# Optimization experiments

Hardware: AMD Instinct MI355X
Metric: run time of the kernel (lower is better)

Reference implementation:

```python
import jax, jax.numpy as jnp
import numpy as np

N_NODES = 50000
N_EDGES = 800000
IN_DIM = 128
IN_CH = 64
HIDDEN = 64
OUT_CH = 128
NUM_CLS = 16
NUM_GRAPHS = 512


def setup_inputs() -> dict:
    key = jax.random.key(0)
    ks = jax.random.split(key, 16)
    s = 0.02
    x = jax.random.normal(ks[0], (N_NODES, IN_DIM), jnp.float32)
    edge_index = jax.random.randint(ks[1], (2, N_EDGES), 0, N_NODES, jnp.int64)
    batch = jnp.sort(jax.random.randint(ks[2], (N_NODES,), 0, NUM_GRAPHS, jnp.int64))
    return {
        "x": x,
        "edge_index": edge_index,
        "batch": batch,
        "num_graphs": NUM_GRAPHS,
        "w_stage1": jax.random.normal(ks[3], (IN_DIM, IN_CH), jnp.float32) * s,
        "b_stage1": jnp.zeros((IN_CH,), jnp.float32),
        "rel1_w": jax.random.normal(ks[4], (IN_CH, HIDDEN), jnp.float32) * s,
        "rel1_b": jnp.zeros((HIDDEN,), jnp.float32),
        "root1_w": jax.random.normal(ks[5], (IN_CH, HIDDEN), jnp.float32) * s,
        "rel2_w": jax.random.normal(ks[6], (HIDDEN, 2 * HIDDEN), jnp.float32) * s,
        "rel2_b": jnp.zeros((2 * HIDDEN,), jnp.float32),
        "root2_w": jax.random.normal(ks[7], (HIDDEN, 2 * HIDDEN), jnp.float32) * s,
        "rel3_w": jax.random.normal(ks[8], (2 * HIDDEN, OUT_CH), jnp.float32) * s,
        "rel3_b": jnp.zeros((OUT_CH,), jnp.float32),
        "root3_w": jax.random.normal(ks[9], (2 * HIDDEN, OUT_CH), jnp.float32) * s,
        "lin_w": jax.random.normal(ks[10], (OUT_CH, NUM_CLS), jnp.float32) * s,
        "lin_b": jnp.zeros((NUM_CLS,), jnp.float32),
    }


def graph_conv(x, src, dst, rel_w, rel_b, root_w, n_nodes):
    # PyG GraphConv(aggr='add'): lin_rel(sum_{j in N(i)} x_j) + lin_root(x_i)
    agg = jax.ops.segment_sum(x[src], dst, num_segments=n_nodes)  # [N, in]
    return agg @ rel_w + rel_b + x @ root_w


def reference(x, edge_index, batch, num_graphs,
              w_stage1, b_stage1,
              rel1_w, rel1_b, root1_w,
              rel2_w, rel2_b, root2_w,
              rel3_w, rel3_b, root3_w,
              lin_w, lin_b):
    src, dst = edge_index[0], edge_index[1]
    n = x.shape[0]
    h = x @ w_stage1 + b_stage1                                   # [N, IN_CH]
    h = jax.nn.relu(graph_conv(h, src, dst, rel1_w, rel1_b, root1_w, n))
    h = jax.nn.relu(graph_conv(h, src, dst, rel2_w, rel2_b, root2_w, n))
    h = jax.nn.relu(graph_conv(h, src, dst, rel3_w, rel3_b, root3_w, n))
    # global mean pool over graphs
    sums = jax.ops.segment_sum(h, batch, num_segments=num_graphs)  # [G, OUT_CH]
    cnt = jax.ops.segment_sum(jnp.ones((n,), h.dtype), batch, num_segments=num_graphs)
    pooled = sums / jnp.maximum(cnt, 1.0)[:, None]
    # dropout treated as identity (deterministic eval reference)
    return pooled @ lin_w + lin_b                                  # [G, NUM_CLS]
```

## Files before the change

kernel.cpp:

```cpp
#include <hip/hip_runtime.h>
#include <hip/hip_bf16.h>

#define N_NODES 50000
#define N_EDGES 800000
#define IN_DIM  128
#define IN_CH   64
#define HIDDEN  64
#define OUT_CH  128
#define NUM_CLS 16
#define NUM_G   512
#define NBUK    ((N_NODES + 255) >> 8)
#define BCAP    6144
#define EPB_A   4096

typedef __attribute__((ext_vector_type(8))) short short8;
typedef __attribute__((ext_vector_type(4))) float f32x4;

__device__ inline float bits2f(unsigned short u) {
  unsigned x = (unsigned)u << 16;
  float f;
  __builtin_memcpy(&f, &x, 4);
  return f;
}
__device__ inline unsigned short f2bits(float v) {
  __hip_bfloat16 b = __float2bfloat16(v);
  unsigned short s;
  __builtin_memcpy(&s, &b, 2);
  return s;
}
__device__ inline short8 zero8() {
  short8 z;
#pragma unroll
  for (int i = 0; i < 8; ++i) z[i] = 0;
  return z;
}
__device__ inline void acc2(float& a0, float& a1, unsigned v) {
  a0 += bits2f((unsigned short)v);
  a1 += bits2f((unsigned short)(v >> 16));
}
__device__ inline void accu4(float* a, uint4 v) {
  acc2(a[0], a[1], v.x); acc2(a[2], a[3], v.y);
  acc2(a[4], a[5], v.z); acc2(a[6], a[7], v.w);
}

__global__ __launch_bounds__(64) void k_stage1(
    const float* __restrict__ Ap, const short* __restrict__ Wa,
    const float* __restrict__ bias, unsigned short* __restrict__ outp) {
  constexpr int DIN = 128, DOUT = 64, KT = DIN / 32, CT = DOUT / 16;
  const int lane = threadIdx.x;
  const int m = lane & 15;
  const int q = lane >> 4;
  const int row = blockIdx.x * 16 + m;
  const bool ok = row < N_NODES;

  short8 afr[KT];
#pragma unroll
  for (int kt = 0; kt < KT; ++kt) {
    short8 f = zero8();
    if (ok) {
      const float* ap = Ap + (size_t)row * DIN + kt * 32 + q * 8;
      float4 x0 = *(const float4*)ap;
      float4 x1 = *(const float4*)(ap + 4);
      f[0] = (short)f2bits(x0.x); f[1] = (short)f2bits(x0.y);
      f[2] = (short)f2bits(x0.z); f[3] = (short)f2bits(x0.w);
      f[4] = (short)f2bits(x1.x); f[5] = (short)f2bits(x1.y);
      f[6] = (short)f2bits(x1.z); f[7] = (short)f2bits(x1.w);
    }
    afr[kt] = f;
  }
  const int rbase = blockIdx.x * 16;
#pragma unroll
  for (int ct = 0; ct < CT; ++ct) {
    f32x4 c = {0.f, 0.f, 0.f, 0.f};
#pragma unroll
    for (int kt = 0; kt < KT; ++kt) {
      short8 b = *(const short8*)(Wa + ((size_t)(kt * CT + ct) * 64 + lane) * 8);
      c = __builtin_amdgcn_mfma_f32_16x16x32_bf16(afr[kt], b, c, 0, 0, 0);
    }
    float bv = bias[ct * 16 + m];
#pragma unroll
    for (int r = 0; r < 4; ++r) {
      int ro = rbase + q * 4 + r;
      if (ro < N_NODES) outp[(size_t)ro * DOUT + ct * 16 + m] = f2bits(c[r] + bv);
    }
  }
}

template <int DIN, int DOUT>
__global__ __launch_bounds__(64) void k_fused(
    const unsigned short* __restrict__ h, const int* __restrict__ esrc,
    const int* __restrict__ off, const short* __restrict__ Wa,
    const short* __restrict__ Wh, const float* __restrict__ bias,
    unsigned short* __restrict__ outp) {
  constexpr int KT = DIN / 32;
  constexpr int CT = DOUT / 16;
  const int lane = threadIdx.x;
  const int m = lane & 15;
  const int q = lane >> 4;
  const int node = blockIdx.x * 16 + m;
  const bool ok = node < N_NODES;

  float acc[KT][8];
#pragma unroll
  for (int kt = 0; kt < KT; ++kt)
#pragma unroll
    for (int j = 0; j < 8; ++j) acc[kt][j] = 0.f;

  if (ok) {
    int e = off[node], end = off[node + 1];
    const unsigned short* hq = h + q * 8;
    for (; e + 2 <= end; e += 2) {
      int s0 = esrc[e], s1 = esrc[e + 1];
      const unsigned short* r0 = hq + (size_t)s0 * DIN;
      const unsigned short* r1 = hq + (size_t)s1 * DIN;
#pragma unroll
      for (int kt = 0; kt < KT; ++kt) {
        uint4 va = *(const uint4*)(r0 + kt * 32);
        uint4 vb = *(const uint4*)(r1 + kt * 32);
        accu4(acc[kt], va);
        accu4(acc[kt], vb);
      }
    }
    if (e < end) {
      const unsigned short* r0 = hq + (size_t)esrc[e] * DIN;
#pragma unroll
      for (int kt = 0; kt < KT; ++kt)
        accu4(acc[kt], *(const uint4*)(r0 + kt * 32));
    }
  }

  short8 afr[KT], hfr[KT];
#pragma unroll
  for (int kt = 0; kt < KT; ++kt) {
    short8 f;
#pragma unroll
    for (int j = 0; j < 8; ++j) f[j] = (short)f2bits(acc[kt][j]);
    afr[kt] = f;
    hfr[kt] = ok ? *(const short8*)(h + (size_t)node * DIN + kt * 32 + q * 8)
                 : zero8();
  }

  const int rbase = blockIdx.x * 16;
#pragma unroll
  for (int ct = 0; ct < CT; ++ct) {
    f32x4 c = {0.f, 0.f, 0.f, 0.f};
#pragma unroll
    for (int kt = 0; kt < KT; ++kt) {
      short8 b = *(const short8*)(Wa + ((size_t)(kt * CT + ct) * 64 + lane) * 8);
      c = __builtin_amdgcn_mfma_f32_16x16x32_bf16(afr[kt], b, c, 0, 0, 0);
      short8 bh = *(const short8*)(Wh + ((size_t)(kt * CT + ct) * 64 + lane) * 8);
      c = __builtin_amdgcn_mfma_f32_16x16x32_bf16(hfr[kt], bh, c, 0, 0, 0);
    }
    float bv = bias[ct * 16 + m];
#pragma unroll
    for (int r = 0; r < 4; ++r) {
      int row = rbase + q * 4 + r;
      if (row < N_NODES)
        outp[(size_t)row * DOUT + ct * 16 + m] = f2bits(fmaxf(c[r] + bv, 0.f));
    }
  }
}

template <int DIN, int DOUT>
__device__ inline void pack1(const float* __restrict__ W, short* __restrict__ o,
                             int t) {
  constexpr int CT = DOUT / 16;
  int j = t & 7;
  int lane = (t >> 3) & 63;
  int kc = t >> 9;
  int ct = kc % CT;
  int kt = kc / CT;
  int k = kt * 32 + (lane >> 4) * 8 + j;
  int n = ct * 16 + (lane & 15);
  o[t] = (short)f2bits(W[k * DOUT + n]);
}

struct PackArgs {
  const float *w1, *r1, *o1, *r2, *o2, *r3, *o3;
  short *w1p, *r1p, *o1p, *r2p, *o2p, *r3p, *o3p;
};

__device__ inline void packflat(const PackArgs& a, int t) {
  if      (t < 8192)  pack1<128, 64>(a.w1, a.w1p, t);
  else if (t < 12288) pack1<64, 64>(a.r1, a.r1p, t - 8192);
  else if (t < 16384) pack1<64, 64>(a.o1, a.o1p, t - 12288);
  else if (t < 24576) pack1<64, 128>(a.r2, a.r2p, t - 16384);
  else if (t < 32768) pack1<64, 128>(a.o2, a.o2p, t - 24576);
  else if (t < 49152) pack1<128, 128>(a.r3, a.r3p, t - 32768);
  else if (t < 65536) pack1<128, 128>(a.o3, a.o3p, t - 49152);
}

__global__ __launch_bounds__(256) void k_bucketA(const int* __restrict__ src,
    const int* __restrict__ dst, int* __restrict__ bcnt, uint2* __restrict__ bbuf,
    PackArgs pk) {
  __shared__ int hist[NBUK], sbase[NBUK], lcur[NBUK];
  const int t = threadIdx.x;

  {
    int g0 = blockIdx.x * 256 + t;
    packflat(pk, g0);
    packflat(pk, g0 + 50176);
  }

  for (int i = t; i < NBUK; i += 256) { hist[i] = 0; lcur[i] = 0; }
  __syncthreads();
  const int e0 = blockIdx.x * EPB_A;
  int s_[16], d_[16];
  int cnt = 0;
#pragma unroll
  for (int k = 0; k < 16; ++k) {
    int e = e0 + k * 256 + t;
    if (e < N_EDGES) {
      s_[cnt] = src[e]; d_[cnt] = dst[e];
      atomicAdd(&hist[d_[cnt] >> 8], 1);
      cnt++;
    }
  }
  __syncthreads();
  for (int i = t; i < NBUK; i += 256) sbase[i] = atomicAdd(&bcnt[i], hist[i]);
  __syncthreads();
  for (int k = 0; k < cnt; ++k) {
    int b = d_[k] >> 8;
    int pos = sbase[b] + atomicAdd(&lcur[b], 1);
    if (pos < BCAP) bbuf[(size_t)b * BCAP + pos] = make_uint2((unsigned)s_[k], (unsigned)d_[k]);
  }
}

__global__ __launch_bounds__(256) void k_bfin(const int* __restrict__ bcnt,
    const uint2* __restrict__ bbuf, int* __restrict__ off,
    int* __restrict__ esrc) {
  __shared__ int cnt[256], s[256], soff[256];
  const int b = blockIdx.x;
  const int t = threadIdx.x;

  int bv0 = (t < NBUK) ? min(bcnt[t], BCAP) : 0;
  s[t] = bv0;
  __syncthreads();
  for (int st = 1; st < 256; st <<= 1) {
    int v = (t >= st) ? s[t - st] : 0;
    __syncthreads();
    s[t] += v;
    __syncthreads();
  }
  __shared__ int bbase_s;
  if (t == b) bbase_s = s[t] - bv0;
  if (b == 0 && t == NBUK - 1) off[N_NODES] = s[t];
  __syncthreads();
  const int bb = bbase_s;

  cnt[t] = 0;
  __syncthreads();
  int n = min(bcnt[b], BCAP);
  for (int i = t; i < n; i += 256)
    atomicAdd(&cnt[bbuf[(size_t)b * BCAP + i].y & 255], 1);
  __syncthreads();
  int v0 = cnt[t];
  s[t] = v0;
  __syncthreads();
  for (int st = 1; st < 256; st <<= 1) {
    int v = (t >= st) ? s[t - st] : 0;
    __syncthreads();
    s[t] += v;
    __syncthreads();
  }
  int myoff = bb + s[t] - v0;
  int node = b * 256 + t;
  if (node < N_NODES) off[node] = myoff;
  soff[t] = myoff;
  cnt[t] = 0;
  __syncthreads();
  for (int i = t; i < n; i += 256) {
    uint2 p = bbuf[(size_t)b * BCAP + i];
    int l = p.y & 255;
    int r = atomicAdd(&cnt[l], 1);
    esrc[soff[l] + r] = (int)p.x;
  }
}

__device__ inline int lbound(const int* __restrict__ a, int n, int v) {
  int lo = 0, hi = n;
  while (lo < hi) {
    int m = (lo + hi) >> 1;
    if (a[m] < v) lo = m + 1; else hi = m;
  }
  return lo;
}

__global__ __launch_bounds__(128) void k_poolhead(const unsigned short* __restrict__ h3,
    const int* __restrict__ batch, const float* __restrict__ lw,
    const float* __restrict__ lb, float* __restrict__ out) {
  __shared__ float sp[128];
  int g = blockIdx.x;
  int t = threadIdx.x;
  int lo = lbound(batch, N_NODES, g);
  int hi = lbound(batch, N_NODES, g + 1);
  float a0 = 0.f, a1 = 0.f, a2 = 0.f, a3 = 0.f;
  int r = lo;
  for (; r + 4 <= hi; r += 4) {
    a0 += bits2f(h3[(size_t)(r + 0) * OUT_CH + t]);
    a1 += bits2f(h3[(size_t)(r + 1) * OUT_CH + t]);
    a2 += bits2f(h3[(size_t)(r + 2) * OUT_CH + t]);
    a3 += bits2f(h3[(size_t)(r + 3) * OUT_CH + t]);
  }
  for (; r < hi; ++r) a0 += bits2f(h3[(size_t)r * OUT_CH + t]);
  float inv = (hi > lo) ? 1.f / (float)(hi - lo) : 0.f;
  sp[t] = ((a0 + a1) + (a2 + a3)) * inv;
  __syncthreads();
  if (t < NUM_CLS) {
    float s = lb[t];
#pragma unroll
    for (int k = 0; k < OUT_CH; ++k) s = fmaf(sp[k], lw[k * NUM_CLS + t], s);
    out[g * NUM_CLS + t] = s;
  }
}

extern "C" void kernel_launch(void* const* d_in, const int* in_sizes, int n_in,
                              void* d_out, int out_size, void* d_ws, size_t ws_size,
                              hipStream_t stream) {
  const float* x      = (const float*)d_in[0];
  const int*   ei     = (const int*)d_in[1];
  const int*   batch  = (const int*)d_in[2];
  const float* w1     = (const float*)d_in[4];
  const float* b1     = (const float*)d_in[5];
  const float* rel1w  = (const float*)d_in[6];
  const float* rel1b  = (const float*)d_in[7];
  const float* root1w = (const float*)d_in[8];
  const float* rel2w  = (const float*)d_in[9];
  const float* rel2b  = (const float*)d_in[10];
  const float* root2w = (const float*)d_in[11];
  const float* rel3w  = (const float*)d_in[12];
  const float* rel3b  = (const float*)d_in[13];
  const float* root3w = (const float*)d_in[14];
  const float* linw   = (const float*)d_in[15];
  const float* linb   = (const float*)d_in[16];
  const int* src = ei;
  const int* dst = ei + N_EDGES;
  float* out = (float*)d_out;

  unsigned short* P = (unsigned short*)d_ws;
  unsigned short* Q = P + (size_t)N_NODES * 128;
  unsigned short* R = Q + (size_t)N_NODES * 128;
  short* WP = (short*)(R + (size_t)N_NODES * 128);
  short* w1p  = WP;
  short* r1p  = w1p + 8192;
  short* o1p  = r1p + 4096;
  short* r2p  = o1p + 4096;
  short* o2p  = r2p + 8192;
  short* r3p  = o2p + 8192;
  short* o3p  = r3p + 16384;
  int* off     = (int*)(o3p + 16384);
  int* bcnt    = off + (N_NODES + 1);
  int* esrc    = bcnt + NBUK + 3;
  uint2* bbuf  = (uint2*)((char*)(esrc + N_EDGES) +
                          ((16 - (((size_t)(esrc + N_EDGES)) & 15)) & 15));

  PackArgs pk = {w1, rel1w, root1w, rel2w, root2w, rel3w, root3w,
                 w1p, r1p, o1p, r2p, o2p, r3p, o3p};

  hipMemsetAsync(bcnt, 0, NBUK * sizeof(int), stream);
  k_bucketA<<<(N_EDGES + EPB_A - 1) / EPB_A, 256, 0, stream>>>(src, dst, bcnt,
                                                               bbuf, pk);
  k_bfin<<<NBUK, 256, 0, stream>>>(bcnt, bbuf, off, esrc);

  const int GF = (N_NODES + 15) / 16;

  k_stage1<<<GF, 64, 0, stream>>>(x, w1p, b1, P);
  k_fused<64, 64><<<GF, 64, 0, stream>>>(P, esrc, off, r1p, o1p, rel1b, R);
  k_fused<64, 128><<<GF, 64, 0, stream>>>(R, esrc, off, r2p, o2p, rel2b, Q);
  k_fused<128, 128><<<GF, 64, 0, stream>>>(Q, esrc, off, r3p, o3p, rel3b, P);
  k_poolhead<<<NUM_G, 128, 0, stream>>>(P, batch, linw, linb, out);
}
```

Measured before the change: 250.5 us.

## Sort nodes by in-degree so GraphConv waves process similar-degree nodes

Adds a degree histogram in k_bfin and a new k_dsort kernel that builds a permutation of nodes ordered by in-degree, in descending order. The fused GraphConv kernels now take their 16 nodes per wave from this permutation and write outputs to the permuted rows. This is meant to cut lane divergence in the neighbor-gather loop, where a wave runs as long as its highest-degree node. In exchange it adds an extra kernel launch and atomics, and it makes the root-feature loads and output stores scattered instead of contiguous.

```diff
diff --git a/kernel.cpp b/kernel.cpp
--- a/kernel.cpp
+++ b/kernel.cpp
@@ -89,16 +89,15 @@
 template <int DIN, int DOUT>
 __global__ __launch_bounds__(64) void k_fused(
     const unsigned short* __restrict__ h, const int* __restrict__ esrc,
-    const int* __restrict__ off, const short* __restrict__ Wa,
-    const short* __restrict__ Wh, const float* __restrict__ bias,
-    unsigned short* __restrict__ outp) {
+    const int* __restrict__ off, const int* __restrict__ perm,
+    const short* __restrict__ Wa, const short* __restrict__ Wh,
+    const float* __restrict__ bias, unsigned short* __restrict__ outp) {
   constexpr int KT = DIN / 32;
   constexpr int CT = DOUT / 16;
   const int lane = threadIdx.x;
   const int m = lane & 15;
   const int q = lane >> 4;
-  const int node = blockIdx.x * 16 + m;
-  const bool ok = node < N_NODES;
+  const int node = perm[blockIdx.x * 16 + m];
 
   float acc[KT][8];
 #pragma unroll
@@ -106,7 +105,7 @@
 #pragma unroll
     for (int j = 0; j < 8; ++j) acc[kt][j] = 0.f;
 
-  if (ok) {
+  {
     int e = off[node], end = off[node + 1];
     const unsigned short* hq = h + q * 8;
     for (; e + 2 <= end; e += 2) {
@@ -136,11 +135,13 @@
 #pragma unroll
     for (int j = 0; j < 8; ++j) f[j] = (short)f2bits(acc[kt][j]);
     afr[kt] = f;
-    hfr[kt] = ok ? *(const short8*)(h + (size_t)node * DIN + kt * 32 + q * 8)
-                 : zero8();
+    hfr[kt] = *(const short8*)(h + (size_t)node * DIN + kt * 32 + q * 8);
   }
 
   const int rbase = blockIdx.x * 16;
+  int prow[4];
+#pragma unroll
+  for (int r = 0; r < 4; ++r) prow[r] = perm[rbase + q * 4 + r];
 #pragma unroll
   for (int ct = 0; ct < CT; ++ct) {
     f32x4 c = {0.f, 0.f, 0.f, 0.f};
@@ -154,9 +155,7 @@
     float bv = bias[ct * 16 + m];
 #pragma unroll
     for (int r = 0; r < 4; ++r) {
-      int row = rbase + q * 4 + r;
-      if (row < N_NODES)
-        outp[(size_t)row * DOUT + ct * 16 + m] = f2bits(fmaxf(c[r] + bv, 0.f));
+      outp[(size_t)prow[r] * DOUT + ct * 16 + m] = f2bits(fmaxf(c[r] + bv, 0.f));
     }
   }
 }
@@ -228,7 +227,7 @@
 
 __global__ __launch_bounds__(256) void k_bfin(const int* __restrict__ bcnt,
     const uint2* __restrict__ bbuf, int* __restrict__ off,
-    int* __restrict__ esrc) {
+    int* __restrict__ esrc, int* __restrict__ ghist) {
   __shared__ int cnt[256], s[256], soff[256];
   const int b = blockIdx.x;
   const int t = threadIdx.x;
@@ -265,7 +264,10 @@
   }
   int myoff = bb + s[t] - v0;
   int node = b * 256 + t;
-  if (node < N_NODES) off[node] = myoff;
+  if (node < N_NODES) {
+    off[node] = myoff;
+    atomicAdd(&ghist[v0 < 255 ? v0 : 255], 1);
+  }
   soff[t] = myoff;
   cnt[t] = 0;
   __syncthreads();
@@ -274,6 +276,29 @@
     int l = p.y & 255;
     int r = atomicAdd(&cnt[l], 1);
     esrc[soff[l] + r] = (int)p.x;
+  }
+}
+
+__global__ __launch_bounds__(256) void k_dsort(const int* __restrict__ off,
+    const int* __restrict__ ghist, int* __restrict__ gcur,
+    int* __restrict__ perm) {
+  __shared__ int s[256];
+  const int t = threadIdx.x;
+  s[t] = ghist[t];
+  __syncthreads();
+  for (int st = 1; st < 256; st <<= 1) {
+    int v = (t + st < 256) ? s[t + st] : 0;
+    __syncthreads();
+    s[t] += v;
+    __syncthreads();
+  }
+  int nid = blockIdx.x * 256 + t;
+  if (nid < N_NODES) {
+    int d = off[nid + 1] - off[nid];
+    if (d > 255) d = 255;
+    int base = (d < 255) ? s[d + 1] : 0;
+    int pos = base + atomicAdd(&gcur[d], 1);
+    perm[pos] = nid;
   }
 }
 
@@ -350,23 +375,27 @@
   short* o3p  = r3p + 16384;
   int* off     = (int*)(o3p + 16384);
   int* bcnt    = off + (N_NODES + 1);
-  int* esrc    = bcnt + NBUK + 3;
+  int* ghist   = bcnt + NBUK;
+  int* gcur    = ghist + 256;
+  int* esrc    = gcur + 256;
   uint2* bbuf  = (uint2*)((char*)(esrc + N_EDGES) +
                           ((16 - (((size_t)(esrc + N_EDGES)) & 15)) & 15));
+  int* perm    = (int*)bbuf;
 
   PackArgs pk = {w1, rel1w, root1w, rel2w, root2w, rel3w, root3w,
                  w1p, r1p, o1p, r2p, o2p, r3p, o3p};
 
-  hipMemsetAsync(bcnt, 0, NBUK * sizeof(int), stream);
+  hipMemsetAsync(bcnt, 0, (NBUK + 512) * sizeof(int), stream);
   k_bucketA<<<(N_EDGES + EPB_A - 1) / EPB_A, 256, 0, stream>>>(src, dst, bcnt,
                                                                bbuf, pk);
-  k_bfin<<<NBUK, 256, 0, stream>>>(bcnt, bbuf, off, esrc);
+  k_bfin<<<NBUK, 256, 0, stream>>>(bcnt, bbuf, off, esrc, ghist);
+  k_dsort<<<(N_NODES + 255) / 256, 256, 0, stream>>>(off, ghist, gcur, perm);
 
   const int GF = (N_NODES + 15) / 16;
 
   k_stage1<<<GF, 64, 0, stream>>>(x, w1p, b1, P);
-  k_fused<64, 64><<<GF, 64, 0, stream>>>(P, esrc, off, r1p, o1p, rel1b, R);
-  k_fused<64, 128><<<GF, 64, 0, stream>>>(R, esrc, off, r2p, o2p, rel2b, Q);
-  k_fused<128, 128><<<GF, 64, 0, stream>>>(Q, esrc, off, r3p, o3p, rel3b, P);
+  k_fused<64, 64><<<GF, 64, 0, stream>>>(P, esrc, off, perm, r1p, o1p, rel1b, R);
+  k_fused<64, 128><<<GF, 64, 0, stream>>>(R, esrc, off, perm, r2p, o2p, rel2b, Q);
+  k_fused<128, 128><<<GF, 64, 0, stream>>>(Q, esrc, off, perm, r3p, o3p, rel3b, P);
   k_poolhead<<<NUM_G, 128, 0, stream>>>(P, batch, linw, linb, out);
 }
```

Measured after the change: 539.5 us. +115.4%, slower.

## Build CSR with global atomic degree count, scan, and atomic scatter

Applied to the files above, without the earlier changes.

Replaces the two-pass bucket sort (shared-memory histograms into a 6144-entry-capped bucket buffer, then per-bucket local sort) with a direct CSR build. The new path counts in-degrees with global atomics, reduces them per 256-node block, scans to get row offsets, and scatters source indices with returned atomic positions. This removes the intermediate bucket buffer and its extra read/write and spreads the work over more blocks. The cost is one more kernel launch plus heavy random global atomics. It also drops the per-row bounds checks in the stage-1 and fused kernels, which is safe only because the node count is an exact multiple of 16.

```diff
diff --git a/kernel.cpp b/kernel.cpp
--- a/kernel.cpp
+++ b/kernel.cpp
@@ -10,8 +10,6 @@
 #define NUM_CLS 16
 #define NUM_G   512
 #define NBUK    ((N_NODES + 255) >> 8)
-#define BCAP    6144
-#define EPB_A   4096
 
 typedef __attribute__((ext_vector_type(8))) short short8;
 typedef __attribute__((ext_vector_type(4))) float f32x4;
@@ -51,21 +49,18 @@
   const int m = lane & 15;
   const int q = lane >> 4;
   const int row = blockIdx.x * 16 + m;
-  const bool ok = row < N_NODES;
 
   short8 afr[KT];
 #pragma unroll
   for (int kt = 0; kt < KT; ++kt) {
-    short8 f = zero8();
-    if (ok) {
-      const float* ap = Ap + (size_t)row * DIN + kt * 32 + q * 8;
-      float4 x0 = *(const float4*)ap;
-      float4 x1 = *(const float4*)(ap + 4);
-      f[0] = (short)f2bits(x0.x); f[1] = (short)f2bits(x0.y);
-      f[2] = (short)f2bits(x0.z); f[3] = (short)f2bits(x0.w);
-      f[4] = (short)f2bits(x1.x); f[5] = (short)f2bits(x1.y);
-      f[6] = (short)f2bits(x1.z); f[7] = (short)f2bits(x1.w);
-    }
+    short8 f;
+    const float* ap = Ap + (size_t)row * DIN + kt * 32 + q * 8;
+    float4 x0 = *(const float4*)ap;
+    float4 x1 = *(const float4*)(ap + 4);
+    f[0] = (short)f2bits(x0.x); f[1] = (short)f2bits(x0.y);
+    f[2] = (short)f2bits(x0.z); f[3] = (short)f2bits(x0.w);
+    f[4] = (short)f2bits(x1.x); f[5] = (short)f2bits(x1.y);
+    f[6] = (short)f2bits(x1.z); f[7] = (short)f2bits(x1.w);
     afr[kt] = f;
   }
   const int rbase = blockIdx.x * 16;
@@ -81,7 +76,7 @@
 #pragma unroll
     for (int r = 0; r < 4; ++r) {
       int ro = rbase + q * 4 + r;
-      if (ro < N_NODES) outp[(size_t)ro * DOUT + ct * 16 + m] = f2bits(c[r] + bv);
+      outp[(size_t)ro * DOUT + ct * 16 + m] = f2bits(c[r] + bv);
     }
   }
 }
@@ -98,7 +93,6 @@
   const int m = lane & 15;
   const int q = lane >> 4;
   const int node = blockIdx.x * 16 + m;
-  const bool ok = node < N_NODES;
 
   float acc[KT][8];
 #pragma unroll
@@ -106,7 +100,7 @@
 #pragma unroll
     for (int j = 0; j < 8; ++j) acc[kt][j] = 0.f;
 
-  if (ok) {
+  {
     int e = off[node], end = off[node + 1];
     const unsigned short* hq = h + q * 8;
     for (; e + 2 <= end; e += 2) {
@@ -136,8 +130,7 @@
 #pragma unroll
     for (int j = 0; j < 8; ++j) f[j] = (short)f2bits(acc[kt][j]);
     afr[kt] = f;
-    hfr[kt] = ok ? *(const short8*)(h + (size_t)node * DIN + kt * 32 + q * 8)
-                 : zero8();
+    hfr[kt] = *(const short8*)(h + (size_t)node * DIN + kt * 32 + q * 8);
   }
 
   const int rbase = blockIdx.x * 16;
@@ -155,8 +148,7 @@
 #pragma unroll
     for (int r = 0; r < 4; ++r) {
       int row = rbase + q * 4 + r;
-      if (row < N_NODES)
-        outp[(size_t)row * DOUT + ct * 16 + m] = f2bits(fmaxf(c[r] + bv, 0.f));
+      outp[(size_t)row * DOUT + ct * 16 + m] = f2bits(fmaxf(c[r] + bv, 0.f));
     }
   }
 }
@@ -190,90 +182,81 @@
   else if (t < 65536) pack1<128, 128>(a.o3, a.o3p, t - 49152);
 }
 
-__global__ __launch_bounds__(256) void k_bucketA(const int* __restrict__ src,
-    const int* __restrict__ dst, int* __restrict__ bcnt, uint2* __restrict__ bbuf,
-    PackArgs pk) {
-  __shared__ int hist[NBUK], sbase[NBUK], lcur[NBUK];
+
+__global__ __launch_bounds__(256) void k_count(const int* __restrict__ dst,
+    int* __restrict__ deg, PackArgs pk) {
   const int t = threadIdx.x;
-
-  {
-    int g0 = blockIdx.x * 256 + t;
-    packflat(pk, g0);
-    packflat(pk, g0 + 50176);
-  }
-
-  for (int i = t; i < NBUK; i += 256) { hist[i] = 0; lcur[i] = 0; }
-  __syncthreads();
-  const int e0 = blockIdx.x * EPB_A;
-  int s_[16], d_[16];
-  int cnt = 0;
-#pragma unroll
-  for (int k = 0; k < 16; ++k) {
+  packflat(pk, blockIdx.x * 256 + t);
+  const int e0 = blockIdx.x * 1024;
+#pragma unroll
+  for (int k = 0; k < 4; ++k) {
+    int e = e0 + k * 256 + t;
+    if (e < N_EDGES) atomicAdd(&deg[dst[e]], 1);
+  }
+}
+
+__global__ __launch_bounds__(256) void k_bsum(const int* __restrict__ deg,
+    int* __restrict__ bcnt) {
+  __shared__ int s[256];
+  const int t = threadIdx.x;
+  const int n = blockIdx.x * 256 + t;
+  s[t] = (n < N_NODES) ? deg[n] : 0;
+  __syncthreads();
+  for (int st = 128; st > 0; st >>= 1) {
+    if (t < st) s[t] += s[t + st];
+    __syncthreads();
+  }
+  if (t == 0) bcnt[blockIdx.x] = s[0];
+}
+
+__global__ __launch_bounds__(256) void k_off(const int* __restrict__ bcnt,
+    const int* __restrict__ deg, int* __restrict__ off, int* __restrict__ cur) {
+  __shared__ int s[256];
+  __shared__ int bbase_s;
+  const int b = blockIdx.x;
+  const int t = threadIdx.x;
+  int bv0 = (t < NBUK) ? bcnt[t] : 0;
+  s[t] = bv0;
+  __syncthreads();
+  for (int st = 1; st < 256; st <<= 1) {
+    int v = (t >= st) ? s[t - st] : 0;
+    __syncthreads();
+    s[t] += v;
+    __syncthreads();
+  }
+  if (t == b) bbase_s = s[t] - bv0;
+  __syncthreads();
+  const int bb = bbase_s;
+
+  const int node = b * 256 + t;
+  int v0 = (node < N_NODES) ? deg[node] : 0;
+  s[t] = v0;
+  __syncthreads();
+  for (int st = 1; st < 256; st <<= 1) {
+    int v = (t >= st) ? s[t - st] : 0;
+    __syncthreads();
+    s[t] += v;
+    __syncthreads();
+  }
+  int myoff = bb + s[t] - v0;
+  if (node < N_NODES) {
+    off[node] = myoff;
+    cur[node] = myoff;
+  }
+  if (b == 0 && t == 0) off[N_NODES] = N_EDGES;
+}
+
+__global__ __launch_bounds__(256) void k_scatter(const int* __restrict__ src,
+    const int* __restrict__ dst, int* __restrict__ cur, int* __restrict__ esrc) {
+  const int t = threadIdx.x;
+  const int e0 = blockIdx.x * 1024;
+#pragma unroll
+  for (int k = 0; k < 4; ++k) {
     int e = e0 + k * 256 + t;
     if (e < N_EDGES) {
-      s_[cnt] = src[e]; d_[cnt] = dst[e];
-      atomicAdd(&hist[d_[cnt] >> 8], 1);
-      cnt++;
-    }
-  }
-  __syncthreads();
-  for (int i = t; i < NBUK; i += 256) sbase[i] = atomicAdd(&bcnt[i], hist[i]);
-  __syncthreads();
-  for (int k = 0; k < cnt; ++k) {
-    int b = d_[k] >> 8;
-    int pos = sbase[b] + atomicAdd(&lcur[b], 1);
-    if (pos < BCAP) bbuf[(size_t)b * BCAP + pos] = make_uint2((unsigned)s_[k], (unsigned)d_[k]);
-  }
-}
-
-__global__ __launch_bounds__(256) void k_bfin(const int* __restrict__ bcnt,
-    const uint2* __restrict__ bbuf, int* __restrict__ off,
-    int* __restrict__ esrc) {
-  __shared__ int cnt[256], s[256], soff[256];
-  const int b = blockIdx.x;
-  const int t = threadIdx.x;
-
-  int bv0 = (t < NBUK) ? min(bcnt[t], BCAP) : 0;
-  s[t] = bv0;
-  __syncthreads();
-  for (int st = 1; st < 256; st <<= 1) {
-    int v = (t >= st) ? s[t - st] : 0;
-    __syncthreads();
-    s[t] += v;
-    __syncthreads();
-  }
-  __shared__ int bbase_s;
-  if (t == b) bbase_s = s[t] - bv0;
-  if (b == 0 && t == NBUK - 1) off[N_NODES] = s[t];
-  __syncthreads();
-  const int bb = bbase_s;
-
-  cnt[t] = 0;
-  __syncthreads();
-  int n = min(bcnt[b], BCAP);
-  for (int i = t; i < n; i += 256)
-    atomicAdd(&cnt[bbuf[(size_t)b * BCAP + i].y & 255], 1);
-  __syncthreads();
-  int v0 = cnt[t];
-  s[t] = v0;
-  __syncthreads();
-  for (int st = 1; st < 256; st <<= 1) {
-    int v = (t >= st) ? s[t - st] : 0;
-    __syncthreads();
-    s[t] += v;
-    __syncthreads();
-  }
-  int myoff = bb + s[t] - v0;
-  int node = b * 256 + t;
-  if (node < N_NODES) off[node] = myoff;
-  soff[t] = myoff;
-  cnt[t] = 0;
-  __syncthreads();
-  for (int i = t; i < n; i += 256) {
-    uint2 p = bbuf[(size_t)b * BCAP + i];
-    int l = p.y & 255;
-    int r = atomicAdd(&cnt[l], 1);
-    esrc[soff[l] + r] = (int)p.x;
+      int pos = atomicAdd(&cur[dst[e]], 1);
+      esrc[pos] = src[e];
+    }
   }
 }
 
@@ -349,18 +332,21 @@
   short* r3p  = o2p + 8192;
   short* o3p  = r3p + 16384;
   int* off     = (int*)(o3p + 16384);
-  int* bcnt    = off + (N_NODES + 1);
-  int* esrc    = bcnt + NBUK + 3;
-  uint2* bbuf  = (uint2*)((char*)(esrc + N_EDGES) +
-                          ((16 - (((size_t)(esrc + N_EDGES)) & 15)) & 15));
+  int* deg     = off + (N_NODES + 1);
+  int* cur     = deg + N_NODES;
+  int* bcnt    = cur + N_NODES;
+  int* esrc    = bcnt + NBUK;
 
   PackArgs pk = {w1, rel1w, root1w, rel2w, root2w, rel3w, root3w,
                  w1p, r1p, o1p, r2p, o2p, r3p, o3p};
 
-  hipMemsetAsync(bcnt, 0, NBUK * sizeof(int), stream);
-  k_bucketA<<<(N_EDGES + EPB_A - 1) / EPB_A, 256, 0, stream>>>(src, dst, bcnt,
-                                                               bbuf, pk);
-  k_bfin<<<NBUK, 256, 0, stream>>>(bcnt, bbuf, off, esrc);
+  const int GE = (N_EDGES + 1023) / 1024;
+
+  hipMemsetAsync(deg, 0, N_NODES * sizeof(int), stream);
+  k_count<<<GE, 256, 0, stream>>>(dst, deg, pk);
+  k_bsum<<<NBUK, 256, 0, stream>>>(deg, bcnt);
+  k_off<<<NBUK, 256, 0, stream>>>(bcnt, deg, off, cur);
+  k_scatter<<<GE, 256, 0, stream>>>(src, dst, cur, esrc);
 
   const int GF = (N_NODES + 15) / 16;
 
```

After: 317.5 us. 1.27x slower.

## Merge stage-1 GEMM into bucket finalize launch and pack bucket entries into 32 bits

Applied to the files above, without the earlier changes.

The stage-1 linear layer now runs as extra blocks (four 16-row waves each) inside the bucket-finalize kernel, which removes one launch and lets the dense GEMM overlap the CSR finalize work. Bucket entries are packed into one 32-bit word (source shifted left by 8, low 8 bits of destination), which halves scratch traffic in both bucket kernels. Bounds checks were dropped in the fused conv kernels because N_NODES is a multiple of 16. The packing relies on source indices fitting in 24 bits.

```diff
diff --git a/kernel.cpp b/kernel.cpp
--- a/kernel.cpp
+++ b/kernel.cpp
@@ -12,6 +12,7 @@
 #define NBUK    ((N_NODES + 255) >> 8)
 #define BCAP    6144
 #define EPB_A   4096
+#define S1BLK   782
 
 typedef __attribute__((ext_vector_type(8))) short short8;
 typedef __attribute__((ext_vector_type(4))) float f32x4;
@@ -43,14 +44,13 @@
   acc2(a[4], a[5], v.z); acc2(a[6], a[7], v.w);
 }
 
-__global__ __launch_bounds__(64) void k_stage1(
-    const float* __restrict__ Ap, const short* __restrict__ Wa,
-    const float* __restrict__ bias, unsigned short* __restrict__ outp) {
+__device__ inline void stage1_wave(const float* __restrict__ Ap,
+    const short* __restrict__ Wa, const float* __restrict__ bias,
+    unsigned short* __restrict__ outp, int rbase, int lane) {
   constexpr int DIN = 128, DOUT = 64, KT = DIN / 32, CT = DOUT / 16;
-  const int lane = threadIdx.x;
   const int m = lane & 15;
   const int q = lane >> 4;
-  const int row = blockIdx.x * 16 + m;
+  const int row = rbase + m;
   const bool ok = row < N_NODES;
 
   short8 afr[KT];
@@ -68,7 +68,6 @@
     }
     afr[kt] = f;
   }
-  const int rbase = blockIdx.x * 16;
 #pragma unroll
   for (int ct = 0; ct < CT; ++ct) {
     f32x4 c = {0.f, 0.f, 0.f, 0.f};
@@ -98,7 +97,6 @@
   const int m = lane & 15;
   const int q = lane >> 4;
   const int node = blockIdx.x * 16 + m;
-  const bool ok = node < N_NODES;
 
   float acc[KT][8];
 #pragma unroll
@@ -106,7 +104,7 @@
 #pragma unroll
     for (int j = 0; j < 8; ++j) acc[kt][j] = 0.f;
 
-  if (ok) {
+  {
     int e = off[node], end = off[node + 1];
     const unsigned short* hq = h + q * 8;
     for (; e + 2 <= end; e += 2) {
@@ -136,8 +134,7 @@
 #pragma unroll
     for (int j = 0; j < 8; ++j) f[j] = (short)f2bits(acc[kt][j]);
     afr[kt] = f;
-    hfr[kt] = ok ? *(const short8*)(h + (size_t)node * DIN + kt * 32 + q * 8)
-                 : zero8();
+    hfr[kt] = *(const short8*)(h + (size_t)node * DIN + kt * 32 + q * 8);
   }
 
   const int rbase = blockIdx.x * 16;
@@ -155,8 +152,7 @@
 #pragma unroll
     for (int r = 0; r < 4; ++r) {
       int row = rbase + q * 4 + r;
-      if (row < N_NODES)
-        outp[(size_t)row * DOUT + ct * 16 + m] = f2bits(fmaxf(c[r] + bv, 0.f));
+      outp[(size_t)row * DOUT + ct * 16 + m] = f2bits(fmaxf(c[r] + bv, 0.f));
     }
   }
 }
@@ -191,8 +187,8 @@
 }
 
 __global__ __launch_bounds__(256) void k_bucketA(const int* __restrict__ src,
-    const int* __restrict__ dst, int* __restrict__ bcnt, uint2* __restrict__ bbuf,
-    PackArgs pk) {
+    const int* __restrict__ dst, int* __restrict__ bcnt,
+    unsigned* __restrict__ bbuf, PackArgs pk) {
   __shared__ int hist[NBUK], sbase[NBUK], lcur[NBUK];
   const int t = threadIdx.x;
 
@@ -222,13 +218,25 @@
   for (int k = 0; k < cnt; ++k) {
     int b = d_[k] >> 8;
     int pos = sbase[b] + atomicAdd(&lcur[b], 1);
-    if (pos < BCAP) bbuf[(size_t)b * BCAP + pos] = make_uint2((unsigned)s_[k], (unsigned)d_[k]);
-  }
-}
-
-__global__ __launch_bounds__(256) void k_bfin(const int* __restrict__ bcnt,
-    const uint2* __restrict__ bbuf, int* __restrict__ off,
-    int* __restrict__ esrc) {
+    if (pos < BCAP)
+      bbuf[(size_t)b * BCAP + pos] =
+          ((unsigned)s_[k] << 8) | ((unsigned)d_[k] & 255u);
+  }
+}
+
+__global__ __launch_bounds__(256) void k_bfin_s1(const int* __restrict__ bcnt,
+    const unsigned* __restrict__ bbuf, int* __restrict__ off,
+    int* __restrict__ esrc,
+    const float* __restrict__ x, const short* __restrict__ w1p,
+    const float* __restrict__ b1, unsigned short* __restrict__ P) {
+  if (blockIdx.x >= NBUK) {
+    const int bs = blockIdx.x - NBUK;
+    const int wave = threadIdx.x >> 6;
+    const int lane = threadIdx.x & 63;
+    stage1_wave(x, w1p, b1, P, bs * 64 + wave * 16, lane);
+    return;
+  }
+
   __shared__ int cnt[256], s[256], soff[256];
   const int b = blockIdx.x;
   const int t = threadIdx.x;
@@ -252,7 +260,7 @@
   __syncthreads();
   int n = min(bcnt[b], BCAP);
   for (int i = t; i < n; i += 256)
-    atomicAdd(&cnt[bbuf[(size_t)b * BCAP + i].y & 255], 1);
+    atomicAdd(&cnt[bbuf[(size_t)b * BCAP + i] & 255u], 1);
   __syncthreads();
   int v0 = cnt[t];
   s[t] = v0;
@@ -270,10 +278,10 @@
   cnt[t] = 0;
   __syncthreads();
   for (int i = t; i < n; i += 256) {
-    uint2 p = bbuf[(size_t)b * BCAP + i];
-    int l = p.y & 255;
+    unsigned p = bbuf[(size_t)b * BCAP + i];
+    int l = (int)(p & 255u);
     int r = atomicAdd(&cnt[l], 1);
-    esrc[soff[l] + r] = (int)p.x;
+    esrc[soff[l] + r] = (int)(p >> 8);
   }
 }
 
@@ -351,8 +359,7 @@
   int* off     = (int*)(o3p + 16384);
   int* bcnt    = off + (N_NODES + 1);
   int* esrc    = bcnt + NBUK + 3;
-  uint2* bbuf  = (uint2*)((char*)(esrc + N_EDGES) +
-                          ((16 - (((size_t)(esrc + N_EDGES)) & 15)) & 15));
+  unsigned* bbuf = (unsigned*)(esrc + N_EDGES);
 
   PackArgs pk = {w1, rel1w, root1w, rel2w, root2w, rel3w, root3w,
                  w1p, r1p, o1p, r2p, o2p, r3p, o3p};
@@ -360,11 +367,11 @@
   hipMemsetAsync(bcnt, 0, NBUK * sizeof(int), stream);
   k_bucketA<<<(N_EDGES + EPB_A - 1) / EPB_A, 256, 0, stream>>>(src, dst, bcnt,
                                                                bbuf, pk);
-  k_bfin<<<NBUK, 256, 0, stream>>>(bcnt, bbuf, off, esrc);
+  k_bfin_s1<<<NBUK + S1BLK, 256, 0, stream>>>(bcnt, bbuf, off, esrc,
+                                              x, w1p, b1, P);
 
   const int GF = (N_NODES + 15) / 16;
 
-  k_stage1<<<GF, 64, 0, stream>>>(x, w1p, b1, P);
   k_fused<64, 64><<<GF, 64, 0, stream>>>(P, esrc, off, r1p, o1p, rel1b, R);
   k_fused<64, 128><<<GF, 64, 0, stream>>>(R, esrc, off, r2p, o2p, rel2b, Q);
   k_fused<128, 128><<<GF, 64, 0, stream>>>(Q, esrc, off, r3p, o3p, rel3b, P);
```

Result: faster. 240.4 us (-4.0%).
